# Kernel optimization log

Measured on AMD Instinct MI355X. Metric: run time of the kernel, lower is better.

Reference implementation:

```python
import jax, jax.numpy as jnp
import numpy as np

B, L, D = 32, 2048, 64
MASK_FILL = -1.0e6  # matches torch code's -1000000.0


def setup_inputs() -> dict:
    key = jax.random.key(0)
    kq, kk, kv, kl = jax.random.split(key, 4)
    queries = jax.random.normal(kq, (B, L, D), dtype=jnp.float32)
    keys = jax.random.normal(kk, (B, L, D), dtype=jnp.float32)
    values = jax.random.normal(kv, (B, L, D), dtype=jnp.float32)
    valid_lens = jax.random.randint(kl, (B,), 1, L + 1, dtype=jnp.int64)
    return {"queries": queries, "keys": keys, "values": values,
            "valid_lens": valid_lens}


def reference(queries, keys, values, valid_lens):
    d = queries.shape[-1]
    # [B, Lq, Lk] scores
    scores = jnp.einsum('bqd,bkd->bqk', queries, keys) / jnp.sqrt(
        jnp.asarray(d, dtype=queries.dtype))
    # length mask: position k valid iff k < valid_lens[b]
    Lk = scores.shape[-1]
    mask = jnp.arange(Lk)[None, :] < valid_lens[:, None]      # [B, Lk]
    scores = jnp.where(mask[:, None, :], scores, MASK_FILL)   # broadcast over Lq
    attn = jax.nn.softmax(scores, axis=-1)
    # dropout p=0.0 -> identity
    return jnp.einsum('bqk,bkv->bqv', attn, values)
```

## Files before the change

kernel.cpp:

```cpp
#include <hip/hip_runtime.h>
#include <hip/hip_bf16.h>
#include <math.h>


#define BB 32
#define LL 2048
#define DD 64
#define QBLK 64
#define KBLK 64
#define NTILES (BB * (LL / QBLK))
#define GRID 768

typedef __attribute__((ext_vector_type(8))) short bf16x8;
typedef __attribute__((ext_vector_type(4))) float f32x4;

static __device__ __forceinline__ short f2bf(float f) {
    __hip_bfloat16 h = __float2bfloat16(f);
    return *reinterpret_cast<short*>(&h);
}
static __device__ __forceinline__ unsigned pk2(float a, float b) {
    return (unsigned)(unsigned short)f2bf(a) | ((unsigned)(unsigned short)f2bf(b) << 16);
}
static __device__ __forceinline__ float exp2c(float x) {
    return __builtin_amdgcn_exp2f(x);
}
static __device__ __forceinline__ int kswz(int row) { return (row & 7) << 3; }
static __device__ __forceinline__ int vswz(int d)   { return ((d ^ (d >> 2)) & 7) << 3; }
static __device__ __forceinline__ int pswz(int row) { return (((row & 7) ^ (row >> 3)) & 7) << 3; }

static __device__ __forceinline__ void cp16(const unsigned short* g,
                                            unsigned short* lbase, int lane) {
#if __has_builtin(__builtin_amdgcn_global_load_lds)
    __builtin_amdgcn_global_load_lds(
        (__attribute__((address_space(1))) void*)g,
        (__attribute__((address_space(3))) void*)lbase, 16, 0, 0);
#else
    *reinterpret_cast<uint4*>(lbase + lane * 8) =
        *reinterpret_cast<const uint4*>(g);
#endif
}

__global__ void init_ctr_kernel(const int* __restrict__ vlen, int* __restrict__ ws) {
    int t = threadIdx.x;
    if (t == 0) ws[0] = 0;
    if (t < BB) {
        int v = vlen[t];
        int rank = 0;
        for (int j = 0; j < BB; ++j) {
            int vj = vlen[j];
            rank += (vj > v) || (vj == v && j < t);
        }
        ws[1 + rank] = t;
    }
}

__global__ __launch_bounds__(256) void convert_kv_kernel(
    const float* __restrict__ K, const float* __restrict__ V,
    unsigned short* __restrict__ kv)
{
    const int tile = blockIdx.x;
    const int tid  = threadIdx.x;
    const float*  Kt  = K + (size_t)tile * (KBLK * DD);
    const float4* Vg4 = reinterpret_cast<const float4*>(V + (size_t)tile * (KBLK * DD));
    unsigned short* img = kv + (size_t)tile * 8192;

    #pragma unroll
    for (int g = 0; g < 2; ++g) {
        int gi = tid + g * 256;
        int kr = gi >> 3;
        int dc = ((gi & 7) * 8) ^ kswz(kr);
        const float4* src = reinterpret_cast<const float4*>(Kt + kr * DD + dc);
        float4 a = src[0], c = src[1];
        uint4 w;
        w.x = pk2(a.x, a.y); w.y = pk2(a.z, a.w);
        w.z = pk2(c.x, c.y); w.w = pk2(c.z, c.w);
        *reinterpret_cast<uint4*>(img + (size_t)gi * 8) = w;
    }

    unsigned short* img2 = img + 4096;
    const int vd4 = (tid & 15) * 4;
    const int vkr = (tid >> 4) * 4;
    float4 v0 = Vg4[(vkr + 0) * 16 + (tid & 15)];
    float4 v1 = Vg4[(vkr + 1) * 16 + (tid & 15)];
    float4 v2 = Vg4[(vkr + 2) * 16 + (tid & 15)];
    float4 v3 = Vg4[(vkr + 3) * 16 + (tid & 15)];
    int e0 = ((vd4 + 0) * 64 + vkr) ^ vswz(vd4 + 0);
    *reinterpret_cast<uint2*>(img2 + e0) = make_uint2(pk2(v0.x, v1.x), pk2(v2.x, v3.x));
    int e1 = ((vd4 + 1) * 64 + vkr) ^ vswz(vd4 + 1);
    *reinterpret_cast<uint2*>(img2 + e1) = make_uint2(pk2(v0.y, v1.y), pk2(v2.y, v3.y));
    int e2 = ((vd4 + 2) * 64 + vkr) ^ vswz(vd4 + 2);
    *reinterpret_cast<uint2*>(img2 + e2) = make_uint2(pk2(v0.z, v1.z), pk2(v2.z, v3.z));
    int e3 = ((vd4 + 3) * 64 + vkr) ^ vswz(vd4 + 3);
    *reinterpret_cast<uint2*>(img2 + e3) = make_uint2(pk2(v0.w, v1.w), pk2(v2.w, v3.w));
}

__global__ __launch_bounds__(256, 2) void attn_mfma_kernel(
    const float* __restrict__ Q, const int* __restrict__ vlen,
    const unsigned short* __restrict__ kvimg,
    float* __restrict__ O, int* __restrict__ ws)
{
    __shared__ __align__(16) unsigned short Ks[2][KBLK * DD];
    __shared__ __align__(16) unsigned short Vt[2][KBLK * DD];
    __shared__ __align__(16) unsigned short Pl[4][16 * KBLK];
    __shared__ int s_tile;

    int* ctr = ws;
    const int* order = ws + 1;

    const int tid  = threadIdx.x;
    const int wid  = tid >> 6;
    const int lane = tid & 63;
    const int lq   = lane & 15;
    const int lg   = lane >> 4;

    const float QSCALE = 0.125f * 1.44269504088896341f;

    for (;;) {
        __syncthreads();
        if (tid == 0) s_tile = atomicAdd(ctr, 1);
        __syncthreads();
        const int tile = s_tile;
        if (tile >= NTILES) break;

        const int b     = order[tile >> 5];
        const int qt    = tile & 31;
        const int qbase = qt * QBLK + wid * 16;
        const int valid = vlen[b];
        const int ntiles = (valid + KBLK - 1) / KBLK;

        const unsigned short* tbase = kvimg + (size_t)b * (32 * 8192);

        auto load_tile = [&](int t, int buf) {
            const unsigned short* tp = tbase + (size_t)t * 8192 + wid * 512 + lane * 8;
            cp16(tp,        &Ks[buf][wid * 512],        lane);
            cp16(tp + 2048, &Ks[buf][2048 + wid * 512], lane);
            cp16(tp + 4096, &Vt[buf][wid * 512],        lane);
            cp16(tp + 6144, &Vt[buf][2048 + wid * 512], lane);
        };

        bf16x8 qf[2];
        {
            const float* Qr = Q + ((size_t)b * LL + qbase + lq) * DD;
            #pragma unroll
            for (int ds_ = 0; ds_ < 2; ++ds_) {
                const float4* p4 = reinterpret_cast<const float4*>(Qr + ds_ * 32 + lg * 8);
                float4 a = p4[0], c = p4[1];
                bf16x8 f;
                f[0] = f2bf(a.x * QSCALE); f[1] = f2bf(a.y * QSCALE);
                f[2] = f2bf(a.z * QSCALE); f[3] = f2bf(a.w * QSCALE);
                f[4] = f2bf(c.x * QSCALE); f[5] = f2bf(c.y * QSCALE);
                f[6] = f2bf(c.z * QSCALE); f[7] = f2bf(c.w * QSCALE);
                qf[ds_] = f;
            }
        }

        f32x4 acc[4];
        #pragma unroll
        for (int n = 0; n < 4; ++n) acc[n] = (f32x4){0.f, 0.f, 0.f, 0.f};
        float m_ = -1e30f, l_ = 0.f;

        load_tile(0, 0);
        __syncthreads();

        for (int kt = 0; kt < ntiles; ++kt) {
            const int cur = kt & 1;

            if (kt + 1 < ntiles) load_tile(kt + 1, cur ^ 1);

            const unsigned short* ks = &Ks[cur][0];
            f32x4 s[4];
            #pragma unroll
            for (int t = 0; t < 4; ++t) {
                f32x4 a = (f32x4){0.f, 0.f, 0.f, 0.f};
                const int krow = t * 16 + lq;
                #pragma unroll
                for (int ds_ = 0; ds_ < 2; ++ds_) {
                    int e = (krow * 64 + ds_ * 32 + lg * 8) ^ kswz(krow);
                    bf16x8 kf = *reinterpret_cast<const bf16x8*>(&ks[e]);
                    a = __builtin_amdgcn_mfma_f32_16x16x32_bf16(kf, qf[ds_], a, 0, 0, 0);
                }
                s[t] = a;
            }

            const bool tail = (kt == ntiles - 1) && (valid & (KBLK - 1));
            if (tail) {
                #pragma unroll
                for (int t = 0; t < 4; ++t)
                    #pragma unroll
                    for (int r = 0; r < 4; ++r) {
                        int kg = kt * KBLK + t * 16 + lg * 4 + r;
                        if (kg >= valid) s[t][r] = -1e30f;
                    }
            }
            float mx = s[0][0];
            #pragma unroll
            for (int t = 0; t < 4; ++t)
                #pragma unroll
                for (int r = 0; r < 4; ++r) mx = fmaxf(mx, s[t][r]);
            mx = fmaxf(mx, __shfl_xor(mx, 16, 64));
            mx = fmaxf(mx, __shfl_xor(mx, 32, 64));

            if (__any(mx - m_ > 8.0f)) {
                float mnew = fmaxf(m_, mx);
                float corr = exp2c(m_ - mnew);
                m_ = mnew;
                l_ *= corr;
                #pragma unroll
                for (int r = 0; r < 4; ++r) {
                    float cq = __shfl(corr, lg * 4 + r, 64);
                    #pragma unroll
                    for (int n = 0; n < 4; ++n) acc[n][r] *= cq;
                }
            }

            float ls = 0.f;
            #pragma unroll
            for (int t = 0; t < 4; ++t)
                #pragma unroll
                for (int r = 0; r < 4; ++r) {
                    float p = exp2c(s[t][r] - m_);
                    s[t][r] = p;
                    ls += p;
                }
            ls += __shfl_xor(ls, 16, 64);
            ls += __shfl_xor(ls, 32, 64);
            l_ += ls;

            unsigned short* Pw = &Pl[wid][0];
            #pragma unroll
            for (int t = 0; t < 4; ++t) {
                int e = (lq * 64 + t * 16 + lg * 4) ^ pswz(lq);
                *reinterpret_cast<uint2*>(&Pw[e]) =
                    make_uint2(pk2(s[t][0], s[t][1]), pk2(s[t][2], s[t][3]));
            }

            const unsigned short* vt = &Vt[cur][0];
            #pragma unroll
            for (int ks_ = 0; ks_ < 2; ++ks_) {
                int pe = (lq * 64 + ks_ * 32 + lg * 8) ^ pswz(lq);
                bf16x8 pf = *reinterpret_cast<const bf16x8*>(&Pw[pe]);
                #pragma unroll
                for (int n = 0; n < 4; ++n) {
                    int drow = n * 16 + lq;
                    int ve = (drow * 64 + ks_ * 32 + lg * 8) ^ vswz(drow);
                    bf16x8 vf = *reinterpret_cast<const bf16x8*>(&vt[ve]);
                    acc[n] = __builtin_amdgcn_mfma_f32_16x16x32_bf16(pf, vf, acc[n], 0, 0, 0);
                }
            }

            __syncthreads();
        }

        float linv[4];
        #pragma unroll
        for (int r = 0; r < 4; ++r)
            linv[r] = 1.f / __shfl(l_, lg * 4 + r, 64);
        float* Ob = O + ((size_t)b * LL + qbase) * DD;
        #pragma unroll
        for (int n = 0; n < 4; ++n) {
            #pragma unroll
            for (int r = 0; r < 4; ++r) {
                Ob[(size_t)(lg * 4 + r) * DD + n * 16 + lq] = acc[n][r] * linv[r];
            }
        }
    }
}

extern "C" void kernel_launch(void* const* d_in, const int* in_sizes, int n_in,
                              void* d_out, int out_size, void* d_ws, size_t ws_size,
                              hipStream_t stream) {
    const float* Q = (const float*)d_in[0];
    const float* K = (const float*)d_in[1];
    const float* V = (const float*)d_in[2];
    const int* vlen = (const int*)d_in[3];
    float* O = (float*)d_out;

    int* ws_i = (int*)d_ws;
    unsigned short* kvimg = (unsigned short*)((char*)d_ws + 1024);

    init_ctr_kernel<<<1, 64, 0, stream>>>(vlen, ws_i);
    convert_kv_kernel<<<BB * (LL / KBLK), 256, 0, stream>>>(K, V, kvimg);
    attn_mfma_kernel<<<GRID, 256, 0, stream>>>(Q, vlen, kvimg, O, ws_i);
}
```

Before: 74.38 us.

## Split attention tile 2x2 across warps over query and key halves

The four warps move from each owning 16 query rows over all 64 keys to a 2x2 grid: each warp owns 32 query rows and one 32-key half of every K/V tile. Each K and V fragment loaded from LDS is now reused for two query subtiles, roughly halving LDS fragment reads per MFMA. Each warp keeps two online-softmax states. At the end, the two key-half partial results are merged through shared memory, with a rescale by the combined max and sum. This adds an extra barrier, LDS staging and exp work in the epilogue, and more registers per thread.

```diff
diff --git a/kernel.cpp b/kernel.cpp
--- a/kernel.cpp
+++ b/kernel.cpp
@@ -102,6 +102,7 @@
     __shared__ __align__(16) unsigned short Ks[2][KBLK * DD];
     __shared__ __align__(16) unsigned short Vt[2][KBLK * DD];
     __shared__ __align__(16) unsigned short Pl[4][16 * KBLK];
+    __shared__ float ml_sh[2][2][32];
     __shared__ int s_tile;
 
     int* ctr = ws;
@@ -112,6 +113,8 @@
     const int lane = tid & 63;
     const int lq   = lane & 15;
     const int lg   = lane >> 4;
+    const int wq   = wid >> 1;
+    const int wk   = wid & 1;
 
     const float QSCALE = 0.125f * 1.44269504088896341f;
 
@@ -124,7 +127,7 @@
 
         const int b     = order[tile >> 5];
         const int qt    = tile & 31;
-        const int qbase = qt * QBLK + wid * 16;
+        const int qbw   = qt * QBLK + wq * 32;
         const int valid = vlen[b];
         const int ntiles = (valid + KBLK - 1) / KBLK;
 
@@ -138,9 +141,10 @@
             cp16(tp + 6144, &Vt[buf][2048 + wid * 512], lane);
         };
 
-        bf16x8 qf[2];
-        {
-            const float* Qr = Q + ((size_t)b * LL + qbase + lq) * DD;
+        bf16x8 qf[2][2];
+        #pragma unroll
+        for (int qsub = 0; qsub < 2; ++qsub) {
+            const float* Qr = Q + ((size_t)b * LL + qbw + qsub * 16 + lq) * DD;
             #pragma unroll
             for (int ds_ = 0; ds_ < 2; ++ds_) {
                 const float4* p4 = reinterpret_cast<const float4*>(Qr + ds_ * 32 + lg * 8);
@@ -150,117 +154,176 @@
                 f[2] = f2bf(a.z * QSCALE); f[3] = f2bf(a.w * QSCALE);
                 f[4] = f2bf(c.x * QSCALE); f[5] = f2bf(c.y * QSCALE);
                 f[6] = f2bf(c.z * QSCALE); f[7] = f2bf(c.w * QSCALE);
-                qf[ds_] = f;
-            }
-        }
-
-        f32x4 acc[4];
+                qf[qsub][ds_] = f;
+            }
+        }
+
+        f32x4 acc[2][4];
         #pragma unroll
-        for (int n = 0; n < 4; ++n) acc[n] = (f32x4){0.f, 0.f, 0.f, 0.f};
-        float m_ = -1e30f, l_ = 0.f;
+        for (int qsub = 0; qsub < 2; ++qsub)
+            #pragma unroll
+            for (int n = 0; n < 4; ++n) acc[qsub][n] = (f32x4){0.f, 0.f, 0.f, 0.f};
+        float m_[2] = {-1e30f, -1e30f}, l_[2] = {0.f, 0.f};
 
         load_tile(0, 0);
         __syncthreads();
 
         for (int kt = 0; kt < ntiles; ++kt) {
             const int cur = kt & 1;
-
             if (kt + 1 < ntiles) load_tile(kt + 1, cur ^ 1);
 
             const unsigned short* ks = &Ks[cur][0];
-            f32x4 s[4];
-            #pragma unroll
-            for (int t = 0; t < 4; ++t) {
-                f32x4 a = (f32x4){0.f, 0.f, 0.f, 0.f};
-                const int krow = t * 16 + lq;
+            bf16x8 kf[2][2];
+            #pragma unroll
+            for (int ksub = 0; ksub < 2; ++ksub) {
+                const int krow = wk * 32 + ksub * 16 + lq;
                 #pragma unroll
                 for (int ds_ = 0; ds_ < 2; ++ds_) {
                     int e = (krow * 64 + ds_ * 32 + lg * 8) ^ kswz(krow);
-                    bf16x8 kf = *reinterpret_cast<const bf16x8*>(&ks[e]);
-                    a = __builtin_amdgcn_mfma_f32_16x16x32_bf16(kf, qf[ds_], a, 0, 0, 0);
-                }
-                s[t] = a;
-            }
+                    kf[ksub][ds_] = *reinterpret_cast<const bf16x8*>(&ks[e]);
+                }
+            }
+
+            f32x4 s[2][2];
+            #pragma unroll
+            for (int qsub = 0; qsub < 2; ++qsub)
+                #pragma unroll
+                for (int ksub = 0; ksub < 2; ++ksub) {
+                    f32x4 a = (f32x4){0.f, 0.f, 0.f, 0.f};
+                    a = __builtin_amdgcn_mfma_f32_16x16x32_bf16(kf[ksub][0], qf[qsub][0], a, 0, 0, 0);
+                    a = __builtin_amdgcn_mfma_f32_16x16x32_bf16(kf[ksub][1], qf[qsub][1], a, 0, 0, 0);
+                    s[qsub][ksub] = a;
+                }
 
             const bool tail = (kt == ntiles - 1) && (valid & (KBLK - 1));
             if (tail) {
-                #pragma unroll
-                for (int t = 0; t < 4; ++t)
+                const int kgb = kt * KBLK + wk * 32;
+                #pragma unroll
+                for (int qsub = 0; qsub < 2; ++qsub)
+                    #pragma unroll
+                    for (int ksub = 0; ksub < 2; ++ksub)
+                        #pragma unroll
+                        for (int r = 0; r < 4; ++r)
+                            if (kgb + ksub * 16 + lg * 4 + r >= valid)
+                                s[qsub][ksub][r] = -1e30f;
+            }
+
+            float mx[2];
+            #pragma unroll
+            for (int qsub = 0; qsub < 2; ++qsub) {
+                float m8 = s[qsub][0][0];
+                #pragma unroll
+                for (int ksub = 0; ksub < 2; ++ksub)
+                    #pragma unroll
+                    for (int r = 0; r < 4; ++r) m8 = fmaxf(m8, s[qsub][ksub][r]);
+                m8 = fmaxf(m8, __shfl_xor(m8, 16, 64));
+                m8 = fmaxf(m8, __shfl_xor(m8, 32, 64));
+                mx[qsub] = m8;
+            }
+
+            float grow = fmaxf(mx[0] - m_[0], mx[1] - m_[1]);
+            if (__any(grow > 8.0f)) {
+                #pragma unroll
+                for (int qsub = 0; qsub < 2; ++qsub) {
+                    float mnew = fmaxf(m_[qsub], mx[qsub]);
+                    float corr = exp2c(m_[qsub] - mnew);
+                    m_[qsub] = mnew;
+                    l_[qsub] *= corr;
                     #pragma unroll
                     for (int r = 0; r < 4; ++r) {
-                        int kg = kt * KBLK + t * 16 + lg * 4 + r;
-                        if (kg >= valid) s[t][r] = -1e30f;
+                        float cq = __shfl(corr, lg * 4 + r, 64);
+                        #pragma unroll
+                        for (int n = 0; n < 4; ++n) acc[qsub][n][r] *= cq;
                     }
-            }
-            float mx = s[0][0];
-            #pragma unroll
-            for (int t = 0; t < 4; ++t)
-                #pragma unroll
-                for (int r = 0; r < 4; ++r) mx = fmaxf(mx, s[t][r]);
-            mx = fmaxf(mx, __shfl_xor(mx, 16, 64));
-            mx = fmaxf(mx, __shfl_xor(mx, 32, 64));
-
-            if (__any(mx - m_ > 8.0f)) {
-                float mnew = fmaxf(m_, mx);
-                float corr = exp2c(m_ - mnew);
-                m_ = mnew;
-                l_ *= corr;
+                }
+            }
+
+            #pragma unroll
+            for (int qsub = 0; qsub < 2; ++qsub) {
+                float ls = 0.f;
+                #pragma unroll
+                for (int ksub = 0; ksub < 2; ++ksub)
+                    #pragma unroll
+                    for (int r = 0; r < 4; ++r) {
+                        float p = exp2c(s[qsub][ksub][r] - m_[qsub]);
+                        s[qsub][ksub][r] = p;
+                        ls += p;
+                    }
+                ls += __shfl_xor(ls, 16, 64);
+                ls += __shfl_xor(ls, 32, 64);
+                l_[qsub] += ls;
+            }
+
+            unsigned short* Pw = &Pl[wid][0];
+            #pragma unroll
+            for (int qsub = 0; qsub < 2; ++qsub)
+                #pragma unroll
+                for (int ksub = 0; ksub < 2; ++ksub) {
+                    int e = (lq * 64 + (qsub * 2 + ksub) * 16 + lg * 4) ^ pswz(lq);
+                    *reinterpret_cast<uint2*>(&Pw[e]) =
+                        make_uint2(pk2(s[qsub][ksub][0], s[qsub][ksub][1]),
+                                   pk2(s[qsub][ksub][2], s[qsub][ksub][3]));
+                }
+
+            const unsigned short* vt = &Vt[cur][0];
+            bf16x8 vf[4];
+            #pragma unroll
+            for (int n = 0; n < 4; ++n) {
+                int drow = n * 16 + lq;
+                int ve = (drow * 64 + wk * 32 + lg * 8) ^ vswz(drow);
+                vf[n] = *reinterpret_cast<const bf16x8*>(&vt[ve]);
+            }
+            #pragma unroll
+            for (int qsub = 0; qsub < 2; ++qsub) {
+                int pe = (lq * 64 + qsub * 32 + lg * 8) ^ pswz(lq);
+                bf16x8 pf = *reinterpret_cast<const bf16x8*>(&Pw[pe]);
+                #pragma unroll
+                for (int n = 0; n < 4; ++n)
+                    acc[qsub][n] = __builtin_amdgcn_mfma_f32_16x16x32_bf16(pf, vf[n], acc[qsub][n], 0, 0, 0);
+            }
+
+            __syncthreads();
+        }
+
+        float* mbuf = (wq == 0) ? (float*)&Ks[0][0] : (float*)&Vt[0][0];
+        if (wk == 1) {
+            #pragma unroll
+            for (int qsub = 0; qsub < 2; ++qsub) {
+                #pragma unroll
+                for (int n = 0; n < 4; ++n)
+                    #pragma unroll
+                    for (int r = 0; r < 4; ++r) {
+                        int ql = qsub * 16 + lg * 4 + r;
+                        mbuf[ql * 65 + n * 16 + lq] = acc[qsub][n][r];
+                    }
+                if (lg == 0) {
+                    ml_sh[wq][0][qsub * 16 + lq] = m_[qsub];
+                    ml_sh[wq][1][qsub * 16 + lq] = l_[qsub];
+                }
+            }
+        }
+        __syncthreads();
+        if (wk == 0) {
+            float* Ob = O + ((size_t)b * LL + qbw) * DD;
+            #pragma unroll
+            for (int qsub = 0; qsub < 2; ++qsub) {
                 #pragma unroll
                 for (int r = 0; r < 4; ++r) {
-                    float cq = __shfl(corr, lg * 4 + r, 64);
-                    #pragma unroll
-                    for (int n = 0; n < 4; ++n) acc[n][r] *= cq;
-                }
-            }
-
-            float ls = 0.f;
-            #pragma unroll
-            for (int t = 0; t < 4; ++t)
-                #pragma unroll
-                for (int r = 0; r < 4; ++r) {
-                    float p = exp2c(s[t][r] - m_);
-                    s[t][r] = p;
-                    ls += p;
-                }
-            ls += __shfl_xor(ls, 16, 64);
-            ls += __shfl_xor(ls, 32, 64);
-            l_ += ls;
-
-            unsigned short* Pw = &Pl[wid][0];
-            #pragma unroll
-            for (int t = 0; t < 4; ++t) {
-                int e = (lq * 64 + t * 16 + lg * 4) ^ pswz(lq);
-                *reinterpret_cast<uint2*>(&Pw[e]) =
-                    make_uint2(pk2(s[t][0], s[t][1]), pk2(s[t][2], s[t][3]));
-            }
-
-            const unsigned short* vt = &Vt[cur][0];
-            #pragma unroll
-            for (int ks_ = 0; ks_ < 2; ++ks_) {
-                int pe = (lq * 64 + ks_ * 32 + lg * 8) ^ pswz(lq);
-                bf16x8 pf = *reinterpret_cast<const bf16x8*>(&Pw[pe]);
-                #pragma unroll
-                for (int n = 0; n < 4; ++n) {
-                    int drow = n * 16 + lq;
-                    int ve = (drow * 64 + ks_ * 32 + lg * 8) ^ vswz(drow);
-                    bf16x8 vf = *reinterpret_cast<const bf16x8*>(&vt[ve]);
-                    acc[n] = __builtin_amdgcn_mfma_f32_16x16x32_bf16(pf, vf, acc[n], 0, 0, 0);
-                }
-            }
-
-            __syncthreads();
-        }
-
-        float linv[4];
-        #pragma unroll
-        for (int r = 0; r < 4; ++r)
-            linv[r] = 1.f / __shfl(l_, lg * 4 + r, 64);
-        float* Ob = O + ((size_t)b * LL + qbase) * DD;
-        #pragma unroll
-        for (int n = 0; n < 4; ++n) {
-            #pragma unroll
-            for (int r = 0; r < 4; ++r) {
-                Ob[(size_t)(lg * 4 + r) * DD + n * 16 + lq] = acc[n][r] * linv[r];
+                    int ql = qsub * 16 + lg * 4 + r;
+                    float m0 = __shfl(m_[qsub], lg * 4 + r, 64);
+                    float l0 = __shfl(l_[qsub], lg * 4 + r, 64);
+                    float m1 = ml_sh[wq][0][ql];
+                    float l1 = ml_sh[wq][1][ql];
+                    float M  = fmaxf(m0, m1);
+                    float w0 = exp2c(m0 - M), w1 = exp2c(m1 - M);
+                    float inv = 1.f / (w0 * l0 + w1 * l1);
+                    #pragma unroll
+                    for (int n = 0; n < 4; ++n) {
+                        float a1 = mbuf[ql * 65 + n * 16 + lq];
+                        Ob[(size_t)ql * DD + n * 16 + lq] =
+                            (w0 * acc[qsub][n][r] + w1 * a1) * inv;
+                    }
+                }
             }
         }
     }
```

After: 78.98 us. 6.2% more time.

## Pre-swizzle KV into MFMA fragment order and software-pipeline QK^T with softmax/PV

Applied to the files above, without the earlier changes.

The conversion kernel now writes K and V in the exact per-lane MFMA fragment layout, so the attention kernel reads fragments linearly without XOR swizzles. The P tile stays in registers and feeds a 16x16x16 bf16 MFMA directly, removing the LDS round-trip for P. A triple-buffered LDS ring lets the QK^T of the next tile overlap the softmax and PV of the current one, with s_setprio raised around MFMA sections. The costs are more register pressure from two score sets, more LDS, and more complex loop control.

```diff
diff --git a/kernel.cpp b/kernel.cpp
--- a/kernel.cpp
+++ b/kernel.cpp
@@ -12,6 +12,7 @@
 #define GRID 768
 
 typedef __attribute__((ext_vector_type(8))) short bf16x8;
+typedef __attribute__((ext_vector_type(4))) short bf16x4;
 typedef __attribute__((ext_vector_type(4))) float f32x4;
 
 static __device__ __forceinline__ short f2bf(float f) {
@@ -24,19 +25,23 @@
 static __device__ __forceinline__ float exp2c(float x) {
     return __builtin_amdgcn_exp2f(x);
 }
-static __device__ __forceinline__ int kswz(int row) { return (row & 7) << 3; }
-static __device__ __forceinline__ int vswz(int d)   { return ((d ^ (d >> 2)) & 7) << 3; }
-static __device__ __forceinline__ int pswz(int row) { return (((row & 7) ^ (row >> 3)) & 7) << 3; }
-
-static __device__ __forceinline__ void cp16(const unsigned short* g,
-                                            unsigned short* lbase, int lane) {
+
+static __device__ __forceinline__ f32x4 mfma16(bf16x4 a, bf16x4 b, f32x4 c) {
+#if __has_builtin(__builtin_amdgcn_mfma_f32_16x16x16bf16_1k)
+    return __builtin_amdgcn_mfma_f32_16x16x16bf16_1k(a, b, c, 0, 0, 0);
+#else
+    asm("v_mfma_f32_16x16x16_bf16 %0, %1, %2, %0" : "+v"(c) : "v"(a), "v"(b));
+    return c;
+#endif
+}
+
+static __device__ __forceinline__ void cp16(const char* g, char* lbase, int lane) {
 #if __has_builtin(__builtin_amdgcn_global_load_lds)
     __builtin_amdgcn_global_load_lds(
         (__attribute__((address_space(1))) void*)g,
         (__attribute__((address_space(3))) void*)lbase, 16, 0, 0);
 #else
-    *reinterpret_cast<uint4*>(lbase + lane * 8) =
-        *reinterpret_cast<const uint4*>(g);
+    *reinterpret_cast<uint4*>(lbase + lane * 16) = *reinterpret_cast<const uint4*>(g);
 #endif
 }
 
@@ -66,32 +71,40 @@
 
     #pragma unroll
     for (int g = 0; g < 2; ++g) {
-        int gi = tid + g * 256;
-        int kr = gi >> 3;
-        int dc = ((gi & 7) * 8) ^ kswz(kr);
-        const float4* src = reinterpret_cast<const float4*>(Kt + kr * DD + dc);
+        int e = tid + g * 256;
+        int f = e >> 6, L = e & 63;
+        int t = f >> 1, ds = f & 1;
+        int lq = L & 15, lg = L >> 4;
+        const float4* src = reinterpret_cast<const float4*>(
+            Kt + (t * 16 + lq) * DD + ds * 32 + lg * 8);
         float4 a = src[0], c = src[1];
         uint4 w;
         w.x = pk2(a.x, a.y); w.y = pk2(a.z, a.w);
         w.z = pk2(c.x, c.y); w.w = pk2(c.z, c.w);
-        *reinterpret_cast<uint4*>(img + (size_t)gi * 8) = w;
+        *reinterpret_cast<uint4*>(img + (size_t)e * 8) = w;
     }
 
     unsigned short* img2 = img + 4096;
     const int vd4 = (tid & 15) * 4;
     const int vkr = (tid >> 4) * 4;
+    const int vt  = vkr >> 4;
+    const int vlg = (vkr >> 2) & 3;
     float4 v0 = Vg4[(vkr + 0) * 16 + (tid & 15)];
     float4 v1 = Vg4[(vkr + 1) * 16 + (tid & 15)];
     float4 v2 = Vg4[(vkr + 2) * 16 + (tid & 15)];
     float4 v3 = Vg4[(vkr + 3) * 16 + (tid & 15)];
-    int e0 = ((vd4 + 0) * 64 + vkr) ^ vswz(vd4 + 0);
-    *reinterpret_cast<uint2*>(img2 + e0) = make_uint2(pk2(v0.x, v1.x), pk2(v2.x, v3.x));
-    int e1 = ((vd4 + 1) * 64 + vkr) ^ vswz(vd4 + 1);
-    *reinterpret_cast<uint2*>(img2 + e1) = make_uint2(pk2(v0.y, v1.y), pk2(v2.y, v3.y));
-    int e2 = ((vd4 + 2) * 64 + vkr) ^ vswz(vd4 + 2);
-    *reinterpret_cast<uint2*>(img2 + e2) = make_uint2(pk2(v0.z, v1.z), pk2(v2.z, v3.z));
-    int e3 = ((vd4 + 3) * 64 + vkr) ^ vswz(vd4 + 3);
-    *reinterpret_cast<uint2*>(img2 + e3) = make_uint2(pk2(v0.w, v1.w), pk2(v2.w, v3.w));
+    const float* p0 = (const float*)&v0;
+    const float* p1 = (const float*)&v1;
+    const float* p2 = (const float*)&v2;
+    const float* p3 = (const float*)&v3;
+    #pragma unroll
+    for (int j = 0; j < 4; ++j) {
+        int col = vd4 + j;
+        int n = col >> 4, lq = col & 15;
+        int L = vlg * 16 + lq;
+        uint2 w = make_uint2(pk2(p0[j], p1[j]), pk2(p2[j], p3[j]));
+        *reinterpret_cast<uint2*>(img2 + (size_t)(n * 4 + vt) * 256 + L * 4) = w;
+    }
 }
 
 __global__ __launch_bounds__(256, 2) void attn_mfma_kernel(
@@ -99,9 +112,7 @@
     const unsigned short* __restrict__ kvimg,
     float* __restrict__ O, int* __restrict__ ws)
 {
-    __shared__ __align__(16) unsigned short Ks[2][KBLK * DD];
-    __shared__ __align__(16) unsigned short Vt[2][KBLK * DD];
-    __shared__ __align__(16) unsigned short Pl[4][16 * KBLK];
+    __shared__ __align__(16) unsigned short Buf[3][8192];
     __shared__ int s_tile;
 
     int* ctr = ws;
@@ -130,12 +141,14 @@
 
         const unsigned short* tbase = kvimg + (size_t)b * (32 * 8192);
 
-        auto load_tile = [&](int t, int buf) {
-            const unsigned short* tp = tbase + (size_t)t * 8192 + wid * 512 + lane * 8;
-            cp16(tp,        &Ks[buf][wid * 512],        lane);
-            cp16(tp + 2048, &Ks[buf][2048 + wid * 512], lane);
-            cp16(tp + 4096, &Vt[buf][wid * 512],        lane);
-            cp16(tp + 6144, &Vt[buf][2048 + wid * 512], lane);
+        auto dma = [&](int t, int bi) {
+            const char* g = (const char*)(tbase + (size_t)t * 8192)
+                            + wid * 4096 + lane * 16;
+            char* l = (char*)&Buf[bi][0] + wid * 4096;
+            cp16(g,        l,        lane);
+            cp16(g + 1024, l + 1024, lane);
+            cp16(g + 2048, l + 2048, lane);
+            cp16(g + 3072, l + 3072, lane);
         };
 
         bf16x8 qf[2];
@@ -159,29 +172,24 @@
         for (int n = 0; n < 4; ++n) acc[n] = (f32x4){0.f, 0.f, 0.f, 0.f};
         float m_ = -1e30f, l_ = 0.f;
 
-        load_tile(0, 0);
-        __syncthreads();
-
-        for (int kt = 0; kt < ntiles; ++kt) {
-            const int cur = kt & 1;
-
-            if (kt + 1 < ntiles) load_tile(kt + 1, cur ^ 1);
-
-            const unsigned short* ks = &Ks[cur][0];
-            f32x4 s[4];
+        auto qkt = [&](int bi, f32x4* s) {
+            const unsigned short* kb = &Buf[bi][0];
+            __builtin_amdgcn_s_setprio(1);
             #pragma unroll
             for (int t = 0; t < 4; ++t) {
                 f32x4 a = (f32x4){0.f, 0.f, 0.f, 0.f};
-                const int krow = t * 16 + lq;
                 #pragma unroll
                 for (int ds_ = 0; ds_ < 2; ++ds_) {
-                    int e = (krow * 64 + ds_ * 32 + lg * 8) ^ kswz(krow);
-                    bf16x8 kf = *reinterpret_cast<const bf16x8*>(&ks[e]);
+                    bf16x8 kf = *reinterpret_cast<const bf16x8*>(
+                        &kb[(size_t)(t * 2 + ds_) * 512 + lane * 8]);
                     a = __builtin_amdgcn_mfma_f32_16x16x32_bf16(kf, qf[ds_], a, 0, 0, 0);
                 }
                 s[t] = a;
             }
-
+            __builtin_amdgcn_s_setprio(0);
+        };
+
+        auto smpv = [&](int kt, f32x4* s, int bi) {
             const bool tail = (kt == ntiles - 1) && (valid & (KBLK - 1));
             if (tail) {
                 #pragma unroll
@@ -226,30 +234,44 @@
             ls += __shfl_xor(ls, 32, 64);
             l_ += ls;
 
-            unsigned short* Pw = &Pl[wid][0];
+            const unsigned short* vb = &Buf[bi][4096];
+            __builtin_amdgcn_s_setprio(1);
             #pragma unroll
             for (int t = 0; t < 4; ++t) {
-                int e = (lq * 64 + t * 16 + lg * 4) ^ pswz(lq);
-                *reinterpret_cast<uint2*>(&Pw[e]) =
-                    make_uint2(pk2(s[t][0], s[t][1]), pk2(s[t][2], s[t][3]));
-            }
-
-            const unsigned short* vt = &Vt[cur][0];
-            #pragma unroll
-            for (int ks_ = 0; ks_ < 2; ++ks_) {
-                int pe = (lq * 64 + ks_ * 32 + lg * 8) ^ pswz(lq);
-                bf16x8 pf = *reinterpret_cast<const bf16x8*>(&Pw[pe]);
+                union { uint2 u; bf16x4 v; } pa;
+                pa.u = make_uint2(pk2(s[t][0], s[t][1]), pk2(s[t][2], s[t][3]));
                 #pragma unroll
                 for (int n = 0; n < 4; ++n) {
-                    int drow = n * 16 + lq;
-                    int ve = (drow * 64 + ks_ * 32 + lg * 8) ^ vswz(drow);
-                    bf16x8 vf = *reinterpret_cast<const bf16x8*>(&vt[ve]);
-                    acc[n] = __builtin_amdgcn_mfma_f32_16x16x32_bf16(pf, vf, acc[n], 0, 0, 0);
+                    union { uint2 u; bf16x4 v; } vv;
+                    vv.u = *reinterpret_cast<const uint2*>(
+                        &vb[(size_t)(n * 4 + t) * 256 + lane * 4]);
+                    acc[n] = mfma16(pa.v, vv.v, acc[n]);
                 }
             }
-
+            __builtin_amdgcn_s_setprio(0);
+        };
+
+        int bc = 0, bn = 1, bd = 2;
+        dma(0, 0);
+        if (ntiles > 1) dma(1, 1);
+        __syncthreads();
+        f32x4 sA[4], sB[4];
+        qkt(0, sA);
+
+        int t = 0;
+        for (; t + 2 <= ntiles; t += 2) {
+            if (t + 2 < ntiles) dma(t + 2, bd);
+            qkt(bn, sB);
+            smpv(t, sA, bc);
             __syncthreads();
+            { int x = bc; bc = bn; bn = bd; bd = x; }
+            if (t + 3 < ntiles) dma(t + 3, bd);
+            if (t + 2 < ntiles) qkt(bn, sA);
+            smpv(t + 1, sB, bc);
+            __syncthreads();
+            { int x = bc; bc = bn; bn = bd; bd = x; }
         }
+        if (t < ntiles) smpv(t, sA, bc);
 
         float linv[4];
         #pragma unroll
```

Result: no change. 74.41 us (+0.1%).
